# Performance work log

Measured on AMD Instinct MI355X. Metric: run time of the kernel, lower is better.

Reference implementation:

```python
import jax, jax.numpy as jnp
import numpy as np

B, N, F, D, H, T = 32, 1024, 32, 64, 64, 4


def setup_inputs() -> dict:
    key = jax.random.key(0)
    ks = jax.random.split(key, 12)
    def w(k, shape):
        return 0.01 * jax.random.normal(k, shape, dtype=jnp.float32)
    z = lambda *s: jnp.zeros(s, jnp.float32)
    return {
        "xv": jax.random.normal(ks[0], (B, N, F), dtype=jnp.float32),
        "option": jax.random.uniform(ks[1], (B, 1), dtype=jnp.float32),
        "adj": jax.random.normal(ks[2], (N, N), dtype=jnp.float32),
        "mu1": w(ks[3], (F, D)),
        "W2": w(ks[4], (D, D)), "b2": z(D),
        "W3": w(ks[5], (D, D)), "b3": z(D),
        "W4": w(ks[6], (D, 1)), "b4": z(D),
        "Wq1": w(ks[7], (D, D)), "bq1": z(D),
        "Wq2": w(ks[8], (D, 1)), "bq2": z(D),
        "Wreg": w(ks[9], (H, 2 * D)), "breg": z(H),
        "Wq": w(ks[10], (1, H)), "bq": z(1),
    }


def reference(xv, option, adj, mu1, W2, b2, W3, b3, W4, b4,
              Wq1, bq1, Wq2, bq2, Wreg, breg, Wq, bq):
    # binary adjacency for message passing, raw weights for the mu_4 branch
    A = (adj > 0).astype(xv.dtype)                       # [N,N]
    mu_1 = jnp.maximum(xv @ mu1, 0.0)                    # [B,N,D]
    # mu_4: Linear(1,D) over every edge weight, clamp, sum over neighbors
    # (identical value every round t>=1, so computed once)
    mu4 = jnp.maximum(adj[..., None] * W4[:, 0] + b4, 0.0).sum(axis=1)[None]  # [1,N,D]
    mu3 = mu4 @ W3.T + b3                                # [1,N,D]
    mu = mu_1                                            # t = 0
    for _ in range(1, T):                                # t = 1..T-1
        mu_pool = jnp.einsum('nm,bmd->bnd', A, mu)       # neighbor aggregation
        mu2 = mu_pool @ W2.T + b2
        mu = jnp.maximum(mu_1 + mu2 + mu3, 0.0)
    mu_mean = jnp.maximum(mu.mean(axis=1, keepdims=True) @ Wq1.T + bq1, 0.0)  # [B,1,D]
    mu_aug = jnp.concatenate([mu, mu_mean], axis=1)      # [B,N+1,D]
    q2 = option.reshape(B, 1, 1) @ Wq2.T + bq2           # [B,1,D]
    q2 = jnp.broadcast_to(q2, (B, N + 1, D))
    q_ = jnp.concatenate([mu_aug, q2], axis=-1)          # [B,N+1,2D]
    qreg = jnp.maximum(q_ @ Wreg.T + breg, 0.0)          # [B,N+1,H]
    return qreg @ Wq.T + bq                              # [B,N+1,1]
```

## Files before the change

kernel.cpp:

```cpp
#include <hip/hip_runtime.h>
#include <hip/hip_bf16.h>

#define Bc 32
#define Nc 1024
#define Fc 32
#define Dc 64
#define Hc 64

typedef __bf16 bf16;
typedef __bf16 bf16x4 __attribute__((ext_vector_type(4)));
typedef __bf16 bf16x8 __attribute__((ext_vector_type(8)));
typedef float  f32x4  __attribute__((ext_vector_type(4)));

#define MS 72
#define PS 68
#define LDS_RND 44032


__global__ void k_init(const float* __restrict__ adj, const float* __restrict__ W4,
                       const float* __restrict__ b4, const float* __restrict__ W3,
                       const float* __restrict__ b3, const float* __restrict__ b2,
                       const float* __restrict__ W2, const float* __restrict__ option,
                       const float* __restrict__ Wq2, const float* __restrict__ bq2,
                       const float* __restrict__ Wreg, const float* __restrict__ breg,
                       const float* __restrict__ xv, const float* __restrict__ mu1w,
                       bf16* __restrict__ Afrag, float* __restrict__ C3,
                       bf16* __restrict__ W2bf, float* __restrict__ c2base,
                       float* __restrict__ musum,
                       float* __restrict__ mu_1, bf16* __restrict__ Xfrag0) {
    const int id = blockIdx.x, t = threadIdx.x;
    __shared__ char smem[39424];
    if (id < 1024) {
        const int n = id;
        float* W3sT  = (float*)smem;
        float* red   = (float*)(smem + 16640);
        float* mu4_s = (float*)(smem + 17664);
        for (int i = t; i < 4096; i += 256)
            W3sT[(i & 63) * 65 + (i >> 6)] = W3[i];
        const float* arow = adj + (size_t)n * Nc;
        {
            const int m0 = t * 4;
            const float4 a = *(const float4*)&arow[m0];
            bf16x4 o;
            o[0] = (bf16)((a.x > 0.f) ? 1.f : 0.f);
            o[1] = (bf16)((a.y > 0.f) ? 1.f : 0.f);
            o[2] = (bf16)((a.z > 0.f) ? 1.f : 0.f);
            o[3] = (bf16)((a.w > 0.f) ? 1.f : 0.f);
            const int g = n >> 4, lm = n & 15;
            const int k0 = m0 >> 5, q = (m0 & 31) >> 3, j = m0 & 7;
            *(bf16x4*)&Afrag[(size_t)((g * 32 + k0) * 64 + lm + 16 * q) * 8 + j] = o;
        }
        const int e = t & 63, g = t >> 6;
        const float w4e = W4[e], b4e = b4[e];
        float acc = 0.f;
        const float4* arow4 = (const float4*)(arow + g * 256);
#pragma unroll 8
        for (int j = 0; j < 64; ++j) {
            const float4 av = arow4[j];
            acc += fmaxf(fmaf(av.x, w4e, b4e), 0.f);
            acc += fmaxf(fmaf(av.y, w4e, b4e), 0.f);
            acc += fmaxf(fmaf(av.z, w4e, b4e), 0.f);
            acc += fmaxf(fmaf(av.w, w4e, b4e), 0.f);
        }
        red[t] = acc;
        __syncthreads();
        if (g == 0) mu4_s[e] = red[e] + red[64 + e] + red[128 + e] + red[192 + e];
        __syncthreads();
        if (t < 64) {
            const int d = t;
            float a = b3[d] + b2[d];
#pragma unroll
            for (int ee = 0; ee < 64; ++ee) a = fmaf(mu4_s[ee], W3sT[ee * 65 + d], a);
            C3[n * 64 + d] = a;
        }
    } else if (id == 1024) {
        for (int j = t * 16; j < t * 16 + 16; ++j) W2bf[j] = (bf16)W2[j];
        for (int i = t; i < 2048; i += 256) musum[i] = 0.f;
        for (int i = t; i < 2048; i += 256) {
            const int b = i >> 6, h = i & 63;
            const float opt = option[b];
            float a = breg[h];
#pragma unroll
            for (int j = 0; j < 64; ++j)
                a = fmaf(fmaf(opt, Wq2[j], bq2[j]), Wreg[h * 128 + 64 + j], a);
            c2base[i] = a;
        }
    } else {
        const int idx = id - 1025, nb = idx & 15, b = idx >> 4;
        const int n0 = nb * 64;
        const int l = t & 63, wv = t >> 6, lm = l & 15, q = l >> 4;
        bf16* W2s = (bf16*)smem;
        bf16* xhi = (bf16*)(smem + 9216);
        bf16* xlo = (bf16*)(smem + 14336);
        bf16* whi = (bf16*)(smem + 19456);
        bf16* wlo = (bf16*)(smem + 24576);
        bf16* muS = (bf16*)(smem + 29696);
        {
            const int row = t >> 2, f0 = (t & 3) * 8;
            const float* src = &xv[((size_t)b * Nc + n0 + row) * Fc + f0];
            const float4 v0 = *(const float4*)src;
            const float4 v1 = *(const float4*)(src + 4);
            bf16x8 hi, lo;
            float vv[8] = {v0.x, v0.y, v0.z, v0.w, v1.x, v1.y, v1.z, v1.w};
#pragma unroll
            for (int j = 0; j < 8; ++j) { hi[j] = (bf16)vv[j]; lo[j] = (bf16)(vv[j] - (float)hi[j]); }
            *(bf16x8*)&xhi[row * 40 + f0] = hi;
            *(bf16x8*)&xlo[row * 40 + f0] = lo;
        }
        {
            const int d = t >> 2, f0 = (t & 3) * 8;
#pragma unroll
            for (int j = 0; j < 8; ++j) {
                const float v = mu1w[(f0 + j) * Dc + d];
                const bf16 hi = (bf16)v;
                whi[d * 40 + f0 + j] = hi;
                wlo[d * 40 + f0 + j] = (bf16)(v - (float)hi);
            }
        }
        {
            const int row = t >> 2, c0 = (t & 3) * 16;
            const float4 v0 = *(const float4*)&W2[row * 64 + c0];
            const float4 v1 = *(const float4*)&W2[row * 64 + c0 + 4];
            const float4 v2 = *(const float4*)&W2[row * 64 + c0 + 8];
            const float4 v3 = *(const float4*)&W2[row * 64 + c0 + 12];
            bf16x8 p0, p1;
            p0[0]=(bf16)v0.x; p0[1]=(bf16)v0.y; p0[2]=(bf16)v0.z; p0[3]=(bf16)v0.w;
            p0[4]=(bf16)v1.x; p0[5]=(bf16)v1.y; p0[6]=(bf16)v1.z; p0[7]=(bf16)v1.w;
            p1[0]=(bf16)v2.x; p1[1]=(bf16)v2.y; p1[2]=(bf16)v2.z; p1[3]=(bf16)v2.w;
            p1[4]=(bf16)v3.x; p1[5]=(bf16)v3.y; p1[6]=(bf16)v3.z; p1[7]=(bf16)v3.w;
            *(bf16x8*)&W2s[row * MS + c0] = p0;
            *(bf16x8*)&W2s[row * MS + c0 + 8] = p1;
        }
        __syncthreads();
        f32x4 acc[4];
#pragma unroll
        for (int ct = 0; ct < 4; ++ct)
#pragma unroll
            for (int r = 0; r < 4; ++r) acc[ct][r] = 0.f;
        {
            const bf16x8 aHi = *(const bf16x8*)&xhi[(wv * 16 + lm) * 40 + q * 8];
            const bf16x8 aLo = *(const bf16x8*)&xlo[(wv * 16 + lm) * 40 + q * 8];
#pragma unroll
            for (int ct = 0; ct < 4; ++ct) {
                const bf16x8 bHi = *(const bf16x8*)&whi[(ct * 16 + lm) * 40 + q * 8];
                const bf16x8 bLo = *(const bf16x8*)&wlo[(ct * 16 + lm) * 40 + q * 8];
                acc[ct] = __builtin_amdgcn_mfma_f32_16x16x32_bf16(aHi, bHi, acc[ct], 0, 0, 0);
                acc[ct] = __builtin_amdgcn_mfma_f32_16x16x32_bf16(aLo, bHi, acc[ct], 0, 0, 0);
                acc[ct] = __builtin_amdgcn_mfma_f32_16x16x32_bf16(aHi, bLo, acc[ct], 0, 0, 0);
            }
        }
#pragma unroll
        for (int ct = 0; ct < 4; ++ct) {
            const int col = ct * 16 + lm;
#pragma unroll
            for (int r = 0; r < 4; ++r) {
                const int row = wv * 16 + q * 4 + r;
                const float v = fmaxf(acc[ct][r], 0.f);
                mu_1[((size_t)b * Nc + n0 + row) * Dc + col] = v;
                muS[row * MS + col] = (bf16)v;
            }
        }
        __syncthreads();
        f32x4 xacc[4];
#pragma unroll
        for (int ct = 0; ct < 4; ++ct)
#pragma unroll
            for (int r = 0; r < 4; ++r) xacc[ct][r] = 0.f;
#pragma unroll
        for (int s = 0; s < 2; ++s) {
            bf16x8 a = *(const bf16x8*)&muS[(wv * 16 + lm) * MS + s * 32 + q * 8];
#pragma unroll
            for (int ct = 0; ct < 4; ++ct) {
                bf16x8 bv = *(const bf16x8*)&W2s[(ct * 16 + lm) * MS + s * 32 + q * 8];
                xacc[ct] = __builtin_amdgcn_mfma_f32_16x16x32_bf16(a, bv, xacc[ct], 0, 0, 0);
            }
        }
        const int k0 = nb * 2 + (wv >> 1);
        const int q_c = (wv & 1) * 2 + (q >> 1);
        const int j0 = (q & 1) * 4;
#pragma unroll
        for (int ct = 0; ct < 4; ++ct) {
            bf16x4 p;
#pragma unroll
            for (int r = 0; r < 4; ++r) p[r] = (bf16)xacc[ct][r];
            *(bf16x4*)&Xfrag0[(size_t)b * 65536
                              + (size_t)((ct * 32 + k0) * 64 + lm + 16 * q_c) * 8 + j0] = p;
        }
    }
}

template <bool FINAL>
__global__ __launch_bounds__(256, 2)
void k_round(const bf16* __restrict__ Afrag, const bf16* __restrict__ Xfr_in,
             const float* __restrict__ mu_1, const float* __restrict__ C3,
             const bf16* __restrict__ W2bf, bf16* __restrict__ Xfr_out,
             const float* __restrict__ Wreg, const float* __restrict__ c2base,
             const float* __restrict__ Wq, const float* __restrict__ bq,
             float* __restrict__ musum, float* __restrict__ out) {
    const int id = blockIdx.x, t = threadIdx.x;
    const int b  = ((id & 7) << 2) | ((id >> 3) & 3);
    const int nb = id >> 5;
    const int n0 = nb * 64;
    const int l = t & 63, wv = t >> 6, lm = l & 15, q = l >> 4;
    const int rh = wv & 1, ch = wv >> 1;
    extern __shared__ char smem[];
    float* part = (float*)smem;
    bf16* WHi   = (bf16*)(smem + 34816);
    bf16* muHi  = (bf16*)smem;
    bf16* muLo  = (bf16*)(smem + 9216);
    bf16* WLo   = (bf16*)(smem + 18432);
    float* rpart = (float*)(smem + 27648);

    if (!FINAL) {
#pragma unroll
        for (int i = 0; i < 2; ++i) {
            int g = i * 256 + t, row = g >> 3, c = g & 7;
            *(bf16x8*)&WHi[row * MS + c * 8] = *(const bf16x8*)&W2bf[row * 64 + c * 8];
        }
    }

    f32x4 acc[4][4];
#pragma unroll
    for (int rt = 0; rt < 4; ++rt)
#pragma unroll
        for (int ct = 0; ct < 4; ++ct)
#pragma unroll
            for (int r = 0; r < 4; ++r) acc[rt][ct][r] = 0.f;

    const bf16* pa[4];
    const bf16* px[4];
#pragma unroll
    for (int g = 0; g < 4; ++g) {
        pa[g] = Afrag + (size_t)(nb * 4 + g) * 16384 + wv * 4096 + l * 8;
        px[g] = Xfr_in + (size_t)b * 65536 + (size_t)g * 16384 + wv * 4096 + l * 8;
    }
#pragma unroll 2
    for (int k = 0; k < 8; ++k) {
        const int o = k * 512;
        bf16x8 a0 = *(const bf16x8*)&pa[0][o];
        bf16x8 a1 = *(const bf16x8*)&pa[1][o];
        bf16x8 a2 = *(const bf16x8*)&pa[2][o];
        bf16x8 a3 = *(const bf16x8*)&pa[3][o];
        bf16x8 x0 = *(const bf16x8*)&px[0][o];
        bf16x8 x1 = *(const bf16x8*)&px[1][o];
        bf16x8 x2 = *(const bf16x8*)&px[2][o];
        bf16x8 x3 = *(const bf16x8*)&px[3][o];
        acc[0][0] = __builtin_amdgcn_mfma_f32_16x16x32_bf16(a0, x0, acc[0][0], 0, 0, 0);
        acc[0][1] = __builtin_amdgcn_mfma_f32_16x16x32_bf16(a0, x1, acc[0][1], 0, 0, 0);
        acc[0][2] = __builtin_amdgcn_mfma_f32_16x16x32_bf16(a0, x2, acc[0][2], 0, 0, 0);
        acc[0][3] = __builtin_amdgcn_mfma_f32_16x16x32_bf16(a0, x3, acc[0][3], 0, 0, 0);
        acc[1][0] = __builtin_amdgcn_mfma_f32_16x16x32_bf16(a1, x0, acc[1][0], 0, 0, 0);
        acc[1][1] = __builtin_amdgcn_mfma_f32_16x16x32_bf16(a1, x1, acc[1][1], 0, 0, 0);
        acc[1][2] = __builtin_amdgcn_mfma_f32_16x16x32_bf16(a1, x2, acc[1][2], 0, 0, 0);
        acc[1][3] = __builtin_amdgcn_mfma_f32_16x16x32_bf16(a1, x3, acc[1][3], 0, 0, 0);
        acc[2][0] = __builtin_amdgcn_mfma_f32_16x16x32_bf16(a2, x0, acc[2][0], 0, 0, 0);
        acc[2][1] = __builtin_amdgcn_mfma_f32_16x16x32_bf16(a2, x1, acc[2][1], 0, 0, 0);
        acc[2][2] = __builtin_amdgcn_mfma_f32_16x16x32_bf16(a2, x2, acc[2][2], 0, 0, 0);
        acc[2][3] = __builtin_amdgcn_mfma_f32_16x16x32_bf16(a2, x3, acc[2][3], 0, 0, 0);
        acc[3][0] = __builtin_amdgcn_mfma_f32_16x16x32_bf16(a3, x0, acc[3][0], 0, 0, 0);
        acc[3][1] = __builtin_amdgcn_mfma_f32_16x16x32_bf16(a3, x1, acc[3][1], 0, 0, 0);
        acc[3][2] = __builtin_amdgcn_mfma_f32_16x16x32_bf16(a3, x2, acc[3][2], 0, 0, 0);
        acc[3][3] = __builtin_amdgcn_mfma_f32_16x16x32_bf16(a3, x3, acc[3][3], 0, 0, 0);
    }

    if (wv < 2) {
#pragma unroll
        for (int rt = 0; rt < 4; ++rt)
#pragma unroll
            for (int ct = 0; ct < 4; ++ct)
                *(f32x4*)&part[(wv * 64 + ct * 16 + lm) * PS + rt * 16 + q * 4] = acc[rt][ct];
    }
    __syncthreads();
    if (wv >= 2) {
#pragma unroll
        for (int rt = 0; rt < 4; ++rt)
#pragma unroll
            for (int ct = 0; ct < 4; ++ct) {
                float* p = &part[((wv - 2) * 64 + ct * 16 + lm) * PS + rt * 16 + q * 4];
                f32x4 v = *(const f32x4*)p;
                *(f32x4*)p = v + acc[rt][ct];
            }
    }
    __syncthreads();
    f32x4 psum[2][2];
#pragma unroll
    for (int rt = 0; rt < 2; ++rt)
#pragma unroll
        for (int ct = 0; ct < 2; ++ct) {
            const int col = ch * 32 + ct * 16 + lm;
            const int row = rh * 32 + rt * 16 + q * 4;
            f32x4 s0 = *(const f32x4*)&part[col * PS + row];
            f32x4 s1 = *(const f32x4*)&part[(64 + col) * PS + row];
            psum[rt][ct] = s0 + s1;
        }

    float vals[2][2][4];
#pragma unroll
    for (int rt = 0; rt < 2; ++rt)
#pragma unroll
        for (int ct = 0; ct < 2; ++ct) {
            const int col = ch * 32 + ct * 16 + lm;
#pragma unroll
            for (int r = 0; r < 4; ++r) {
                const int n = n0 + rh * 32 + rt * 16 + q * 4 + r;
                float v = mu_1[((size_t)b * Nc + n) * Dc + col] + psum[rt][ct][r]
                        + C3[n * 64 + col];
                vals[rt][ct][r] = fmaxf(v, 0.f);
            }
        }
    if (FINAL) {
#pragma unroll
        for (int ct = 0; ct < 2; ++ct) {
            float s = 0.f;
#pragma unroll
            for (int rt = 0; rt < 2; ++rt)
#pragma unroll
                for (int r = 0; r < 4; ++r) s += vals[rt][ct][r];
            s += __shfl_xor(s, 16);
            s += __shfl_xor(s, 32);
            if (q == 0) atomicAdd(&musum[b * 64 + ch * 32 + ct * 16 + lm], s);
        }
    }
    __syncthreads();

#pragma unroll
    for (int rt = 0; rt < 2; ++rt)
#pragma unroll
        for (int ct = 0; ct < 2; ++ct) {
            const int col = ch * 32 + ct * 16 + lm;
#pragma unroll
            for (int r = 0; r < 4; ++r) {
                const int row = rh * 32 + rt * 16 + q * 4 + r;
                const float v = vals[rt][ct][r];
                const bf16 hi = (bf16)v;
                muHi[row * MS + col] = hi;
                if (FINAL) muLo[row * MS + col] = (bf16)(v - (float)hi);
            }
        }
    if (FINAL) {
#pragma unroll
        for (int i = 0; i < 4; ++i) {
            int g = i * 1024 + t * 4, h = g >> 6, d = g & 63;
            const float4 w4 = *(const float4*)&Wreg[h * 128 + d];
            bf16x4 ohi, olo;
            ohi[0] = (bf16)w4.x; olo[0] = (bf16)(w4.x - (float)ohi[0]);
            ohi[1] = (bf16)w4.y; olo[1] = (bf16)(w4.y - (float)ohi[1]);
            ohi[2] = (bf16)w4.z; olo[2] = (bf16)(w4.z - (float)ohi[2]);
            ohi[3] = (bf16)w4.w; olo[3] = (bf16)(w4.w - (float)ohi[3]);
            *(bf16x4*)&WHi[h * MS + d] = ohi;
            *(bf16x4*)&WLo[h * MS + d] = olo;
        }
    }
    __syncthreads();

    f32x4 xacc[2][2];
#pragma unroll
    for (int rt = 0; rt < 2; ++rt)
#pragma unroll
        for (int ct = 0; ct < 2; ++ct)
#pragma unroll
            for (int r = 0; r < 4; ++r) xacc[rt][ct][r] = 0.f;

    if (!FINAL) {
#pragma unroll
        for (int s = 0; s < 2; ++s) {
            bf16x8 aM[2], bW[2];
#pragma unroll
            for (int rt = 0; rt < 2; ++rt)
                aM[rt] = *(const bf16x8*)&muHi[(rh * 32 + rt * 16 + lm) * MS + s * 32 + q * 8];
#pragma unroll
            for (int ct = 0; ct < 2; ++ct)
                bW[ct] = *(const bf16x8*)&WHi[(ch * 32 + ct * 16 + lm) * MS + s * 32 + q * 8];
#pragma unroll
            for (int rt = 0; rt < 2; ++rt)
#pragma unroll
                for (int ct = 0; ct < 2; ++ct)
                    xacc[rt][ct] = __builtin_amdgcn_mfma_f32_16x16x32_bf16(aM[rt], bW[ct],
                                                                           xacc[rt][ct], 0, 0, 0);
        }
        const int k0 = nb * 2 + rh;
        const int q_c0 = (q >> 1), j0 = (q & 1) * 4;
#pragma unroll
        for (int rt = 0; rt < 2; ++rt)
#pragma unroll
            for (int ct = 0; ct < 2; ++ct) {
                bf16x4 p;
#pragma unroll
                for (int r = 0; r < 4; ++r) p[r] = (bf16)xacc[rt][ct][r];
                *(bf16x4*)&Xfr_out[(size_t)b * 65536
                    + (size_t)(((ch * 2 + ct) * 32 + k0) * 64 + lm + 16 * (rt * 2 + q_c0)) * 8
                    + j0] = p;
            }
    } else {
#pragma unroll
        for (int s = 0; s < 2; ++s) {
            bf16x8 aH[2], aL[2], bH[2], bL[2];
#pragma unroll
            for (int rt = 0; rt < 2; ++rt) {
                const int ao = (rh * 32 + rt * 16 + lm) * MS + s * 32 + q * 8;
                aH[rt] = *(const bf16x8*)&muHi[ao];
                aL[rt] = *(const bf16x8*)&muLo[ao];
            }
#pragma unroll
            for (int ct = 0; ct < 2; ++ct) {
                const int bo = (ch * 32 + ct * 16 + lm) * MS + s * 32 + q * 8;
                bH[ct] = *(const bf16x8*)&WHi[bo];
                bL[ct] = *(const bf16x8*)&WLo[bo];
            }
#pragma unroll
            for (int rt = 0; rt < 2; ++rt)
#pragma unroll
                for (int ct = 0; ct < 2; ++ct) {
                    xacc[rt][ct] = __builtin_amdgcn_mfma_f32_16x16x32_bf16(aH[rt], bH[ct],
                                                                           xacc[rt][ct], 0, 0, 0);
                    xacc[rt][ct] = __builtin_amdgcn_mfma_f32_16x16x32_bf16(aL[rt], bH[ct],
                                                                           xacc[rt][ct], 0, 0, 0);
                    xacc[rt][ct] = __builtin_amdgcn_mfma_f32_16x16x32_bf16(aH[rt], bL[ct],
                                                                           xacc[rt][ct], 0, 0, 0);
                }
        }
        const float bq0 = bq[0];
        float rowsum[2][4] = {{0.f, 0.f, 0.f, 0.f}, {0.f, 0.f, 0.f, 0.f}};
#pragma unroll
        for (int ct = 0; ct < 2; ++ct) {
            const int h = ch * 32 + ct * 16 + lm;
            const float c2 = c2base[b * 64 + h];
            const float wqh = Wq[h];
#pragma unroll
            for (int rt = 0; rt < 2; ++rt)
#pragma unroll
                for (int r = 0; r < 4; ++r)
                    rowsum[rt][r] += fmaxf(xacc[rt][ct][r] + c2, 0.f) * wqh;
        }
#pragma unroll
        for (int rt = 0; rt < 2; ++rt)
#pragma unroll
            for (int r = 0; r < 4; ++r) {
                float v = rowsum[rt][r];
                v += __shfl_xor(v, 1);
                v += __shfl_xor(v, 2);
                v += __shfl_xor(v, 4);
                v += __shfl_xor(v, 8);
                if (lm == 0) rpart[ch * 64 + rh * 32 + rt * 16 + q * 4 + r] = v;
            }
        __syncthreads();
        if (t < 64)
            out[(size_t)b * (Nc + 1) + n0 + t] = rpart[t] + rpart[64 + t] + bq0;
    }
}

__global__ void k_tail(const float* __restrict__ musum, const float* __restrict__ Wq1,
                       const float* __restrict__ bq1, const float* __restrict__ Wreg,
                       const float* __restrict__ c2base, const float* __restrict__ Wq,
                       const float* __restrict__ bq, float* __restrict__ out) {
    const int b = blockIdx.x, l = threadIdx.x;
    __shared__ float mean_s[64];
    __shared__ float mp[64];
    mean_s[l] = musum[b * 64 + l] * (1.f / Nc);
    __syncthreads();
    float a = bq1[l];
#pragma unroll
    for (int e = 0; e < 64; ++e) a = fmaf(mean_s[e], Wq1[l * 64 + e], a);
    mp[l] = fmaxf(a, 0.f);
    __syncthreads();
    float h = c2base[b * 64 + l];
#pragma unroll
    for (int d = 0; d < 64; ++d) h = fmaf(mp[d], Wreg[l * 128 + d], h);
    float v = fmaxf(h, 0.f) * Wq[l];
#pragma unroll
    for (int off = 32; off; off >>= 1) v += __shfl_down(v, off);
    if (l == 0) out[(size_t)b * (Nc + 1) + Nc] = v + bq[0];
}

extern "C" void kernel_launch(void* const* d_in, const int* in_sizes, int n_in,
                              void* d_out, int out_size, void* d_ws, size_t ws_size,
                              hipStream_t stream) {
    const float* xv     = (const float*)d_in[0];
    const float* option = (const float*)d_in[1];
    const float* adj    = (const float*)d_in[2];
    const float* mu1w   = (const float*)d_in[3];
    const float* W2     = (const float*)d_in[4];
    const float* b2     = (const float*)d_in[5];
    const float* W3     = (const float*)d_in[6];
    const float* b3     = (const float*)d_in[7];
    const float* W4     = (const float*)d_in[8];
    const float* b4     = (const float*)d_in[9];
    const float* Wq1    = (const float*)d_in[10];
    const float* bq1    = (const float*)d_in[11];
    const float* Wq2    = (const float*)d_in[12];
    const float* bq2    = (const float*)d_in[13];
    const float* Wreg   = (const float*)d_in[14];
    const float* breg   = (const float*)d_in[15];
    const float* Wq     = (const float*)d_in[16];
    const float* bq     = (const float*)d_in[17];
    float* out = (float*)d_out;

    float* ws = (float*)d_ws;
    const size_t MU = (size_t)Bc * Nc * Dc;
    float* mu_1     = ws;
    float* C3       = ws + MU;
    float* c2base   = C3 + 65536;
    float* musum    = c2base + 2048;
    bf16*  Afrag    = (bf16*)(musum + 2048);
    bf16*  W2bf     = Afrag + (size_t)Nc * Nc;
    bf16*  Xf0      = W2bf + 4096;
    bf16*  Xf1      = Xf0 + MU;

    k_init<<<1537, 256, 0, stream>>>(adj, W4, b4, W3, b3, b2, W2, option, Wq2, bq2,
                                     Wreg, breg, xv, mu1w,
                                     Afrag, C3, W2bf, c2base, musum, mu_1, Xf0);
    k_round<false><<<512, 256, LDS_RND, stream>>>(
        Afrag, Xf0, mu_1, C3, W2bf, Xf1,
        nullptr, nullptr, nullptr, nullptr, nullptr, nullptr);
    k_round<false><<<512, 256, LDS_RND, stream>>>(
        Afrag, Xf1, mu_1, C3, W2bf, Xf0,
        nullptr, nullptr, nullptr, nullptr, nullptr, nullptr);
    k_round<true><<<512, 256, LDS_RND, stream>>>(
        Afrag, Xf0, mu_1, C3, nullptr, nullptr,
        Wreg, c2base, Wq, bq, musum, out);
    k_tail<<<Bc, 64, 0, stream>>>(musum, Wq1, bq1, Wreg, c2base, Wq, bq, out);
}
```

Measured before the change: 146.4 us.

## Fuse tail into final round via last-block atomic counter; rebalance init grid

Removes the separate k_tail launch. Each block of the final round increments an atomic counter, and the last block to finish computes the mean-pooled head for all 32 batches. Separately, k_init now puts the mu_1 blocks first and has each adjacency block process two rows, shrinking the grid from 1537 to 1025 blocks. This saves one launch and spreads the adj work more evenly, but the serial tail work now runs on a single block and relies on the counter ordering being correct.

```diff
diff --git a/kernel.cpp b/kernel.cpp
--- a/kernel.cpp
+++ b/kernel.cpp
@@ -27,66 +27,12 @@
                        bf16* __restrict__ Afrag, float* __restrict__ C3,
                        bf16* __restrict__ W2bf, float* __restrict__ c2base,
                        float* __restrict__ musum,
-                       float* __restrict__ mu_1, bf16* __restrict__ Xfrag0) {
+                       float* __restrict__ mu_1, bf16* __restrict__ Xfrag0,
+                       unsigned* __restrict__ done) {
     const int id = blockIdx.x, t = threadIdx.x;
     __shared__ char smem[39424];
-    if (id < 1024) {
-        const int n = id;
-        float* W3sT  = (float*)smem;
-        float* red   = (float*)(smem + 16640);
-        float* mu4_s = (float*)(smem + 17664);
-        for (int i = t; i < 4096; i += 256)
-            W3sT[(i & 63) * 65 + (i >> 6)] = W3[i];
-        const float* arow = adj + (size_t)n * Nc;
-        {
-            const int m0 = t * 4;
-            const float4 a = *(const float4*)&arow[m0];
-            bf16x4 o;
-            o[0] = (bf16)((a.x > 0.f) ? 1.f : 0.f);
-            o[1] = (bf16)((a.y > 0.f) ? 1.f : 0.f);
-            o[2] = (bf16)((a.z > 0.f) ? 1.f : 0.f);
-            o[3] = (bf16)((a.w > 0.f) ? 1.f : 0.f);
-            const int g = n >> 4, lm = n & 15;
-            const int k0 = m0 >> 5, q = (m0 & 31) >> 3, j = m0 & 7;
-            *(bf16x4*)&Afrag[(size_t)((g * 32 + k0) * 64 + lm + 16 * q) * 8 + j] = o;
-        }
-        const int e = t & 63, g = t >> 6;
-        const float w4e = W4[e], b4e = b4[e];
-        float acc = 0.f;
-        const float4* arow4 = (const float4*)(arow + g * 256);
-#pragma unroll 8
-        for (int j = 0; j < 64; ++j) {
-            const float4 av = arow4[j];
-            acc += fmaxf(fmaf(av.x, w4e, b4e), 0.f);
-            acc += fmaxf(fmaf(av.y, w4e, b4e), 0.f);
-            acc += fmaxf(fmaf(av.z, w4e, b4e), 0.f);
-            acc += fmaxf(fmaf(av.w, w4e, b4e), 0.f);
-        }
-        red[t] = acc;
-        __syncthreads();
-        if (g == 0) mu4_s[e] = red[e] + red[64 + e] + red[128 + e] + red[192 + e];
-        __syncthreads();
-        if (t < 64) {
-            const int d = t;
-            float a = b3[d] + b2[d];
-#pragma unroll
-            for (int ee = 0; ee < 64; ++ee) a = fmaf(mu4_s[ee], W3sT[ee * 65 + d], a);
-            C3[n * 64 + d] = a;
-        }
-    } else if (id == 1024) {
-        for (int j = t * 16; j < t * 16 + 16; ++j) W2bf[j] = (bf16)W2[j];
-        for (int i = t; i < 2048; i += 256) musum[i] = 0.f;
-        for (int i = t; i < 2048; i += 256) {
-            const int b = i >> 6, h = i & 63;
-            const float opt = option[b];
-            float a = breg[h];
-#pragma unroll
-            for (int j = 0; j < 64; ++j)
-                a = fmaf(fmaf(opt, Wq2[j], bq2[j]), Wreg[h * 128 + 64 + j], a);
-            c2base[i] = a;
-        }
-    } else {
-        const int idx = id - 1025, nb = idx & 15, b = idx >> 4;
+    if (id < 512) {
+        const int nb = id & 15, b = id >> 4;
         const int n0 = nb * 64;
         const int l = t & 63, wv = t >> 6, lm = l & 15, q = l >> 4;
         bf16* W2s = (bf16*)smem;
@@ -186,6 +132,65 @@
             *(bf16x4*)&Xfrag0[(size_t)b * 65536
                               + (size_t)((ct * 32 + k0) * 64 + lm + 16 * q_c) * 8 + j0] = p;
         }
+    } else if (id < 1024) {
+        const int ar = id - 512;
+        float* W3sT  = (float*)smem;
+        float* red   = (float*)(smem + 16640);
+        float* mu4_s = (float*)(smem + 17664);
+        for (int i = t; i < 4096; i += 256)
+            W3sT[(i & 63) * 65 + (i >> 6)] = W3[i];
+        for (int rr = 0; rr < 2; ++rr) {
+            const int n = ar * 2 + rr;
+            const float* arow = adj + (size_t)n * Nc;
+            {
+                const int m0 = t * 4;
+                const float4 a = *(const float4*)&arow[m0];
+                bf16x4 o;
+                o[0] = (bf16)((a.x > 0.f) ? 1.f : 0.f);
+                o[1] = (bf16)((a.y > 0.f) ? 1.f : 0.f);
+                o[2] = (bf16)((a.z > 0.f) ? 1.f : 0.f);
+                o[3] = (bf16)((a.w > 0.f) ? 1.f : 0.f);
+                const int g = n >> 4, lm = n & 15;
+                const int k0 = m0 >> 5, qq = (m0 & 31) >> 3, j = m0 & 7;
+                *(bf16x4*)&Afrag[(size_t)((g * 32 + k0) * 64 + lm + 16 * qq) * 8 + j] = o;
+            }
+            const int e = t & 63, g = t >> 6;
+            const float w4e = W4[e], b4e = b4[e];
+            float acc = 0.f;
+            const float4* arow4 = (const float4*)(arow + g * 256);
+#pragma unroll 8
+            for (int j = 0; j < 64; ++j) {
+                const float4 av = arow4[j];
+                acc += fmaxf(fmaf(av.x, w4e, b4e), 0.f);
+                acc += fmaxf(fmaf(av.y, w4e, b4e), 0.f);
+                acc += fmaxf(fmaf(av.z, w4e, b4e), 0.f);
+                acc += fmaxf(fmaf(av.w, w4e, b4e), 0.f);
+            }
+            red[t] = acc;
+            __syncthreads();
+            if (g == 0) mu4_s[e] = red[e] + red[64 + e] + red[128 + e] + red[192 + e];
+            __syncthreads();
+            if (t < 64) {
+                float a = b3[t] + b2[t];
+#pragma unroll
+                for (int ee = 0; ee < 64; ++ee) a = fmaf(mu4_s[ee], W3sT[ee * 65 + t], a);
+                C3[n * 64 + t] = a;
+            }
+            __syncthreads();
+        }
+    } else {
+        for (int j = t * 16; j < t * 16 + 16; ++j) W2bf[j] = (bf16)W2[j];
+        for (int i = t; i < 2048; i += 256) musum[i] = 0.f;
+        if (t < 16) done[t] = 0u;
+        for (int i = t; i < 2048; i += 256) {
+            const int b = i >> 6, h = i & 63;
+            const float opt = option[b];
+            float a = breg[h];
+#pragma unroll
+            for (int j = 0; j < 64; ++j)
+                a = fmaf(fmaf(opt, Wq2[j], bq2[j]), Wreg[h * 128 + 64 + j], a);
+            c2base[i] = a;
+        }
     }
 }
 
@@ -196,7 +201,9 @@
              const bf16* __restrict__ W2bf, bf16* __restrict__ Xfr_out,
              const float* __restrict__ Wreg, const float* __restrict__ c2base,
              const float* __restrict__ Wq, const float* __restrict__ bq,
-             float* __restrict__ musum, float* __restrict__ out) {
+             const float* __restrict__ Wq1, const float* __restrict__ bq1,
+             float* __restrict__ musum, float* __restrict__ out,
+             unsigned* __restrict__ done) {
     const int id = blockIdx.x, t = threadIdx.x;
     const int b  = ((id & 7) << 2) | ((id >> 3) & 3);
     const int nb = id >> 5;
@@ -204,6 +211,7 @@
     const int l = t & 63, wv = t >> 6, lm = l & 15, q = l >> 4;
     const int rh = wv & 1, ch = wv >> 1;
     extern __shared__ char smem[];
+    __shared__ unsigned last_s;
     float* part = (float*)smem;
     bf16* WHi   = (bf16*)(smem + 34816);
     bf16* muHi  = (bf16*)smem;
@@ -446,30 +454,49 @@
         __syncthreads();
         if (t < 64)
             out[(size_t)b * (Nc + 1) + n0 + t] = rpart[t] + rpart[64 + t] + bq0;
-    }
-}
-
-__global__ void k_tail(const float* __restrict__ musum, const float* __restrict__ Wq1,
-                       const float* __restrict__ bq1, const float* __restrict__ Wreg,
-                       const float* __restrict__ c2base, const float* __restrict__ Wq,
-                       const float* __restrict__ bq, float* __restrict__ out) {
-    const int b = blockIdx.x, l = threadIdx.x;
-    __shared__ float mean_s[64];
-    __shared__ float mp[64];
-    mean_s[l] = musum[b * 64 + l] * (1.f / Nc);
-    __syncthreads();
-    float a = bq1[l];
-#pragma unroll
-    for (int e = 0; e < 64; ++e) a = fmaf(mean_s[e], Wq1[l * 64 + e], a);
-    mp[l] = fmaxf(a, 0.f);
-    __syncthreads();
-    float h = c2base[b * 64 + l];
-#pragma unroll
-    for (int d = 0; d < 64; ++d) h = fmaf(mp[d], Wreg[l * 128 + d], h);
-    float v = fmaxf(h, 0.f) * Wq[l];
-#pragma unroll
-    for (int off = 32; off; off >>= 1) v += __shfl_down(v, off);
-    if (l == 0) out[(size_t)b * (Nc + 1) + Nc] = v + bq[0];
+
+        asm volatile("s_waitcnt vmcnt(0)" ::: "memory");
+        __syncthreads();
+        if (t == 0) {
+            const unsigned old =
+                __hip_atomic_fetch_add(done, 1u, __ATOMIC_RELAXED, __HIP_MEMORY_SCOPE_AGENT);
+            last_s = (old == 511u) ? 1u : 0u;
+        }
+        __syncthreads();
+        if (last_s) {
+            float* Wq1T   = (float*)smem;
+            float* WrT    = (float*)(smem + 16640);
+            float* mean_s = (float*)(smem + 33280);
+            float* mp     = (float*)(smem + 34304);
+            for (int i = t; i < 4096; i += 256) {
+                const int rI = i >> 6, cI = i & 63;
+                Wq1T[cI * 65 + rI] = Wq1[i];
+                WrT[cI * 65 + rI]  = Wreg[rI * 128 + cI];
+            }
+            __syncthreads();
+            const int sb = t >> 6, d = t & 63;
+            for (int bb = 0; bb < Bc; bb += 4) {
+                const int bT = bb + sb;
+                mean_s[sb * 64 + d] =
+                    __hip_atomic_load(&musum[bT * 64 + d],
+                                      __ATOMIC_RELAXED, __HIP_MEMORY_SCOPE_AGENT) * (1.f / Nc);
+                __syncthreads();
+                float a = bq1[d];
+#pragma unroll
+                for (int e = 0; e < 64; ++e) a = fmaf(mean_s[sb * 64 + e], Wq1T[e * 65 + d], a);
+                mp[sb * 64 + d] = fmaxf(a, 0.f);
+                __syncthreads();
+                float h = c2base[bT * 64 + d];
+#pragma unroll
+                for (int e = 0; e < 64; ++e) h = fmaf(mp[sb * 64 + e], WrT[e * 65 + d], h);
+                float v = fmaxf(h, 0.f) * Wq[d];
+#pragma unroll
+                for (int off = 32; off; off >>= 1) v += __shfl_down(v, off);
+                if (d == 0) out[(size_t)bT * (Nc + 1) + Nc] = v + bq0;
+                __syncthreads();
+            }
+        }
+    }
 }
 
 extern "C" void kernel_launch(void* const* d_in, const int* in_sizes, int n_in,
@@ -501,22 +528,22 @@
     float* C3       = ws + MU;
     float* c2base   = C3 + 65536;
     float* musum    = c2base + 2048;
-    bf16*  Afrag    = (bf16*)(musum + 2048);
+    unsigned* done  = (unsigned*)(musum + 2048);
+    bf16*  Afrag    = (bf16*)(done + 16);
     bf16*  W2bf     = Afrag + (size_t)Nc * Nc;
     bf16*  Xf0      = W2bf + 4096;
     bf16*  Xf1      = Xf0 + MU;
 
-    k_init<<<1537, 256, 0, stream>>>(adj, W4, b4, W3, b3, b2, W2, option, Wq2, bq2,
+    k_init<<<1025, 256, 0, stream>>>(adj, W4, b4, W3, b3, b2, W2, option, Wq2, bq2,
                                      Wreg, breg, xv, mu1w,
-                                     Afrag, C3, W2bf, c2base, musum, mu_1, Xf0);
+                                     Afrag, C3, W2bf, c2base, musum, mu_1, Xf0, done);
     k_round<false><<<512, 256, LDS_RND, stream>>>(
         Afrag, Xf0, mu_1, C3, W2bf, Xf1,
-        nullptr, nullptr, nullptr, nullptr, nullptr, nullptr);
+        nullptr, nullptr, nullptr, nullptr, nullptr, nullptr, nullptr, nullptr, nullptr);
     k_round<false><<<512, 256, LDS_RND, stream>>>(
         Afrag, Xf1, mu_1, C3, W2bf, Xf0,
-        nullptr, nullptr, nullptr, nullptr, nullptr, nullptr);
+        nullptr, nullptr, nullptr, nullptr, nullptr, nullptr, nullptr, nullptr, nullptr);
     k_round<true><<<512, 256, LDS_RND, stream>>>(
         Afrag, Xf0, mu_1, C3, nullptr, nullptr,
-        Wreg, c2base, Wq, bq, musum, out);
-    k_tail<<<Bc, 64, 0, stream>>>(musum, Wq1, bq1, Wreg, c2base, Wq, bq, out);
+        Wreg, c2base, Wq, bq, Wq1, bq1, musum, out, done);
 }
```

Result: slower. 173.6 us (+18.6%).
